# Kernel tuning notes

Hardware: AMD Instinct MI355X
Metric: run time of the kernel (lower is better)

## Reference

```python
import jax, jax.numpy as jnp
import numpy as np

B, M = 4, 32768            # scenes, candidate slots
A = B * (M // 2)           # static number of active points per group
CINS = (64, 128)           # per-group input channels
HID, COUT = 128, 256       # cfg.mlps = [128, 256]
EPS = 1e-5                 # BatchNorm eps


def setup_inputs() -> dict:
    key = jax.random.key(0)
    ks = jax.random.split(key, 12)
    # hard mask: first M//2 columns of every row active -> exactly A True entries
    mask = jnp.tile(jnp.arange(M) < (M // 2), (B, 1))
    inp = {
        "feats0": jax.random.normal(ks[0], (CINS[0], A), jnp.float32),
        "feats1": jax.random.normal(ks[1], (CINS[1], A), jnp.float32),
        "prob0": jax.random.uniform(ks[2], (B, M), jnp.float32),
        "prob1": jax.random.uniform(ks[3], (B, M), jnp.float32),
        "mask0": mask,
        "mask1": mask,
    }
    for g, cin in enumerate(CINS):
        inp[f"Wa{g}"] = jax.random.normal(ks[4 + 2 * g], (HID, cin), jnp.float32) * 0.05
        inp[f"ga{g}"] = jnp.ones((HID,), jnp.float32)
        inp[f"ba{g}"] = jnp.zeros((HID,), jnp.float32)
        inp[f"Wb{g}"] = jax.random.normal(ks[5 + 2 * g], (COUT, HID), jnp.float32) * 0.05
        inp[f"gb{g}"] = jnp.ones((COUT,), jnp.float32)
        inp[f"bb{g}"] = jnp.zeros((COUT,), jnp.float32)
    return inp


def _bn_relu(x, gamma, beta):
    # training-mode BatchNorm1d over the length axis (N=1), biased variance like torch
    mu = x.mean(axis=1, keepdims=True)
    var = x.var(axis=1, keepdims=True)
    y = (x - mu) * jax.lax.rsqrt(var + EPS) * gamma[:, None] + beta[:, None]
    return jax.nn.relu(y)


def _group(feats, prob, mask, Wa, ga, ba, Wb, gb, bb):
    # 1x1 Conv1d == matmul over channels
    h = _bn_relu(Wa @ feats, ga, ba)          # (HID, A)
    y = _bn_relu(Wb @ h, gb, bb)              # (COUT, A)
    # masked scatter into dense (COUT, B*M) zero tensor, row-major like torch bool indexing
    idx = jnp.nonzero(mask.reshape(-1), size=A)[0]
    full = jnp.zeros((COUT, B * M), y.dtype).at[:, idx].set(y)
    # training-time soft-mask weighting by prob, broadcast over channels
    return full.reshape(COUT, B, M) * prob[None]


def reference(feats0, feats1, prob0, prob1, mask0, mask1,
              Wa0, ga0, ba0, Wb0, gb0, bb0,
              Wa1, ga1, ba1, Wb1, gb1, bb1):
    f0 = _group(feats0, prob0, mask0, Wa0, ga0, ba0, Wb0, gb0, bb0)
    f1 = _group(feats1, prob1, mask1, Wa1, ga1, ba1, Wb1, gb1, bb1)
    # sum over groups, then (C,B,M) -> (B,C,M)
    return (f0 + f1).transpose(1, 0, 2)
```

## Files before the change

kernel.cpp:

```cpp
#include <hip/hip_runtime.h>


#define AT 65536

typedef __bf16 bf16_t;
typedef bf16_t bf16x8 __attribute__((ext_vector_type(8)));
typedef bf16_t bf16x4 __attribute__((ext_vector_type(4)));
typedef float  f32x4  __attribute__((ext_vector_type(4)));

__device__ __forceinline__ f32x4 mfma16(bf16x8 a, bf16x8 b, f32x4 c) {
  return __builtin_amdgcn_mfma_f32_16x16x32_bf16(a, b, c, 0, 0, 0);
}

__device__ __forceinline__ float redcol16(float v) {
  v += __shfl_xor(v, 1, 64);
  v += __shfl_xor(v, 2, 64);
  v += __shfl_xor(v, 4, 64);
  v += __shfl_xor(v, 8, 64);
  return v;
}

__device__ __forceinline__ float mux4(const float* v, int sel) {
  float r = v[0];
  r = (sel == 1) ? v[1] : r;
  r = (sel == 2) ? v[2] : r;
  r = (sel == 3) ? v[3] : r;
  return r;
}

__global__ __launch_bounds__(256) void prep_weights(
    const float* __restrict__ Wa0, const float* __restrict__ Wa1,
    const float* __restrict__ Wb0, const float* __restrict__ Wb1,
    bf16_t* __restrict__ Wab0, bf16_t* __restrict__ Wab1,
    bf16_t* __restrict__ Wbb0, bf16_t* __restrict__ Wbb1,
    float* __restrict__ stats)
{
  const int i = threadIdx.x + blockIdx.x * 256;
  if (i < 8192)        Wab0[i]         = (bf16_t)Wa0[i];
  else if (i < 24576)  Wab1[i - 8192]  = (bf16_t)Wa1[i - 8192];
  else if (i < 57344)  Wbb0[i - 24576] = (bf16_t)Wb0[i - 24576];
  else if (i < 90112)  Wbb1[i - 57344] = (bf16_t)Wb1[i - 57344];
  else if (i < 91648)  stats[i - 90112] = 0.f;
}

template <int CIN>
__device__ __forceinline__ void trans_one(
    const float* __restrict__ feats, const bf16_t* __restrict__ Wab,
    float* __restrict__ zsum, float* __restrict__ zssq,
    bf16_t* __restrict__ fT, int blk, char* __restrict__ tile)
{
  constexpr int KS1  = CIN / 32;
  constexpr int GR   = CIN / 8;
  constexpr int ROWB = CIN * 2;
  const int tid = threadIdx.x, lane = tid & 63;
  const int lr = lane & 15, lk = lane >> 4, wid = tid >> 6;
  const int a0 = blk * 64;

  f32x4 v[CIN / 16];
  const int cb = tid >> 4, aq = (tid & 15) * 4;
#pragma unroll
  for (int cc = 0; cc < CIN / 16; ++cc)
    v[cc] = *reinterpret_cast<const f32x4*>(
        feats + (size_t)(cc * 16 + cb) * AT + a0 + aq);

#pragma unroll
  for (int cc = 0; cc < CIN / 16; ++cc) {
    const int c = cc * 16 + cb;
    const int gsw = c >> 3, cbyte = (c & 7) * 2;
#pragma unroll
    for (int i = 0; i < 4; ++i) {
      const int a = aq + i;
      *reinterpret_cast<bf16_t*>(
          tile + a * ROWB + ((gsw ^ (a & 7)) << 4) + cbyte) = (bf16_t)v[cc][i];
    }
  }
  __syncthreads();

  {
    const int g = tid % GR, ar = tid / GR;
#pragma unroll
    for (int i = 0; i < (GR * 64) / 256; ++i) {
      const int a = ar + (256 / GR) * i;
      const bf16x8 w = *reinterpret_cast<const bf16x8*>(
          tile + a * ROWB + ((g ^ (a & 7)) << 4));
      *reinterpret_cast<bf16x8*>(fT + (size_t)(a0 + a) * CIN + g * 8) = w;
    }
  }

  bf16x8 WaF[2][KS1];
#pragma unroll
  for (int mi = 0; mi < 2; ++mi) {
    const bf16_t* base = Wab + (size_t)((2 * wid + mi) * 16 + lr) * CIN + lk * 8;
#pragma unroll
    for (int ks = 0; ks < KS1; ++ks)
      WaF[mi][ks] = *reinterpret_cast<const bf16x8*>(base + ks * 32);
  }

  float zs[2][4] = {}, zq[2][4] = {};
#pragma unroll
  for (int nt = 0; nt < 4; ++nt) {
    const int col = lr + 16 * nt;
    f32x4 z0 = {0.f, 0.f, 0.f, 0.f}, z1 = {0.f, 0.f, 0.f, 0.f};
#pragma unroll
    for (int ks = 0; ks < KS1; ++ks) {
      const int g2 = ks * 4 + lk;
      const bf16x8 bfr = *reinterpret_cast<const bf16x8*>(
          tile + col * ROWB + ((g2 ^ (col & 7)) << 4));
      z0 = mfma16(WaF[0][ks], bfr, z0);
      z1 = mfma16(WaF[1][ks], bfr, z1);
    }
#pragma unroll
    for (int i = 0; i < 4; ++i) {
      zs[0][i] += z0[i]; zq[0][i] += z0[i] * z0[i];
      zs[1][i] += z1[i]; zq[1][i] += z1[i] * z1[i];
    }
  }
#pragma unroll
  for (int mi = 0; mi < 2; ++mi) {
#pragma unroll
    for (int i = 0; i < 4; ++i) {
      zs[mi][i] = redcol16(zs[mi][i]);
      zq[mi][i] = redcol16(zq[mi][i]);
    }
    const float vs = mux4(zs[mi], lr & 3);
    const float vq = mux4(zq[mi], lr & 3);
    const float vv = (lr & 4) ? vq : vs;
    if (lr < 8) {
      const int ch = (2 * wid + mi) * 16 + lk * 4 + (lr & 3);
      atomicAdd(((lr & 4) ? zssq : zsum) + ch, vv);
    }
  }
}

__global__ __launch_bounds__(256) void trans_stats_all(
    const float* __restrict__ feats0, const float* __restrict__ feats1,
    const bf16_t* __restrict__ Wab0, const bf16_t* __restrict__ Wab1,
    float* __restrict__ zsum, float* __restrict__ zssq,
    bf16_t* __restrict__ fT0, bf16_t* __restrict__ fT1)
{
  __shared__ __align__(16) char tile[64 * 256];
  if (blockIdx.x < 1024)
    trans_one<64>(feats0, Wab0, zsum, zssq, fT0, blockIdx.x, tile);
  else
    trans_one<128>(feats1, Wab1, zsum + 128, zssq + 128, fT1,
                   blockIdx.x - 1024, tile);
}

__global__ void finalize_stats(const float* __restrict__ sum,
                               const float* __restrict__ ssq,
                               const float* __restrict__ gamma0,
                               const float* __restrict__ beta0,
                               const float* __restrict__ gamma1,
                               const float* __restrict__ beta1,
                               float* __restrict__ scale,
                               float* __restrict__ shift, int nch)
{
  const int t = threadIdx.x;
  const int g = t / nch;
  const int c = t - g * nch;
  const float inv = 1.f / 65536.f;
  const float mu  = sum[t] * inv;
  const float var = ssq[t] * inv - mu * mu;
  const float ga  = (g ? gamma1 : gamma0)[c];
  const float be  = (g ? beta1 : beta0)[c];
  const float sc  = ga * rsqrtf(var + 1e-5f);
  scale[t] = sc;
  shift[t] = be - mu * sc;
}

template <int CIN>
__device__ __forceinline__ void gemm1_dev(
    const bf16_t* __restrict__ fT, const bf16_t* __restrict__ Wab,
    const float* __restrict__ scZ, const float* __restrict__ shZ,
    char* __restrict__ hw, int colbase, int lr, int lk)
{
  constexpr int KS = CIN / 32;

  bf16x8 bf[2][KS];
#pragma unroll
  for (int sub = 0; sub < 2; ++sub)
#pragma unroll
    for (int ks = 0; ks < KS; ++ks)
      bf[sub][ks] = *reinterpret_cast<const bf16x8*>(
          fT + (size_t)(colbase + sub * 16 + lr) * CIN + lk * 8 + ks * 32);

#pragma unroll 2
  for (int rb = 0; rb < 8; ++rb) {
    bf16x8 af[KS];
    const bf16_t* wa = Wab + (size_t)(rb * 16 + lr) * CIN + lk * 8;
#pragma unroll
    for (int ks = 0; ks < KS; ++ks)
      af[ks] = *reinterpret_cast<const bf16x8*>(wa + ks * 32);

    f32x4 acc[2];
    acc[0] = f32x4{0.f, 0.f, 0.f, 0.f};
    acc[1] = f32x4{0.f, 0.f, 0.f, 0.f};
#pragma unroll
    for (int ks = 0; ks < KS; ++ks) {
      acc[0] = mfma16(af[ks], bf[0][ks], acc[0]);
      acc[1] = mfma16(af[ks], bf[1][ks], acc[1]);
    }

    const f32x4 sv = *reinterpret_cast<const f32x4*>(scZ + rb * 16 + lk * 4);
    const f32x4 bv = *reinterpret_cast<const f32x4*>(shZ + rb * 16 + lk * 4);
#pragma unroll
    for (int sub = 0; sub < 2; ++sub) {
      bf16x4 hv;
#pragma unroll
      for (int i = 0; i < 4; ++i)
        hv[i] = (bf16_t)fmaxf(acc[sub][i] * sv[i] + bv[i], 0.f);
      const int col = sub * 16 + lr;
      const int g8  = rb * 2 + (lk >> 1);
      *reinterpret_cast<bf16x4*>(
          hw + col * 256 + ((g8 ^ (col & 7)) << 4) + ((lk & 1) << 3)) = hv;
    }
  }
}

template <int PHASE>
__global__ __launch_bounds__(256) void fused_pass(
    const bf16_t* __restrict__ fT0, const bf16_t* __restrict__ fT1,
    const bf16_t* __restrict__ Wab0, const bf16_t* __restrict__ Wab1,
    const bf16_t* __restrict__ Wbb0, const bf16_t* __restrict__ Wbb1,
    const float* __restrict__ prob0, const float* __restrict__ prob1,
    const float* __restrict__ scaleZ, const float* __restrict__ shiftZ,
    const float* __restrict__ scaleY, const float* __restrict__ shiftY,
    float* __restrict__ ysum, float* __restrict__ yssq,
    float* __restrict__ out)
{
  __shared__ __align__(16) char hbuf[4][2][8192];
  __shared__ float sstat[(PHASE == 2) ? 1024 : 4];

  const int tid = threadIdx.x, wid = tid >> 6, lane = tid & 63;
  const int lr = lane & 15, lk = lane >> 4;
  const int colbase = (int)blockIdx.x * 128 + wid * 32;

  if constexpr (PHASE == 2) {
    sstat[tid] = 0.f; sstat[tid + 256] = 0.f;
    sstat[tid + 512] = 0.f; sstat[tid + 768] = 0.f;
  }

  gemm1_dev<64>(fT0, Wab0, scaleZ, shiftZ, &hbuf[wid][0][0], colbase, lr, lk);
  gemm1_dev<128>(fT1, Wab1, scaleZ + 128, shiftZ + 128, &hbuf[wid][1][0],
                 colbase, lr, lk);

  if constexpr (PHASE == 2) __syncthreads();

  float p0v[2] = {0.f, 0.f}, p1v[2] = {0.f, 0.f};
  const int bC = (colbase >> 14) * 256;
  const int m0 = colbase & 16383;
  if constexpr (PHASE == 3) {
    const int b = colbase >> 14;
#pragma unroll
    for (int sub = 0; sub < 2; ++sub) {
      const int mm = m0 + sub * 16 + lr;
      p0v[sub] = prob0[((size_t)b << 15) + mm];
      p1v[sub] = prob1[((size_t)b << 15) + mm];
    }
  }

#pragma unroll 2
  for (int rb2 = 0; rb2 < 16; ++rb2) {
    bf16x8 a0f[4], a1f[4];
    const bf16_t* w0 = Wbb0 + (size_t)(rb2 * 16 + lr) * 128 + lk * 8;
    const bf16_t* w1 = Wbb1 + (size_t)(rb2 * 16 + lr) * 128 + lk * 8;
#pragma unroll
    for (int ks = 0; ks < 4; ++ks) {
      a0f[ks] = *reinterpret_cast<const bf16x8*>(w0 + ks * 32);
      a1f[ks] = *reinterpret_cast<const bf16x8*>(w1 + ks * 32);
    }

    f32x4 acc0[2], acc1[2];
    acc0[0] = f32x4{0.f, 0.f, 0.f, 0.f}; acc0[1] = f32x4{0.f, 0.f, 0.f, 0.f};
    acc1[0] = f32x4{0.f, 0.f, 0.f, 0.f}; acc1[1] = f32x4{0.f, 0.f, 0.f, 0.f};
#pragma unroll
    for (int ks2 = 0; ks2 < 4; ++ks2) {
#pragma unroll
      for (int sub = 0; sub < 2; ++sub) {
        const int col = sub * 16 + lr;
        const int off = col * 256 + (((ks2 * 4 + lk) ^ (col & 7)) << 4);
        const bf16x8 h0 = *reinterpret_cast<const bf16x8*>(&hbuf[wid][0][0] + off);
        acc0[sub] = mfma16(a0f[ks2], h0, acc0[sub]);
        const bf16x8 h1 = *reinterpret_cast<const bf16x8*>(&hbuf[wid][1][0] + off);
        acc1[sub] = mfma16(a1f[ks2], h1, acc1[sub]);
      }
    }

    if constexpr (PHASE == 2) {
#pragma unroll
      for (int g = 0; g < 2; ++g) {
        const f32x4* ac = g ? acc1 : acc0;
        float s[4], q[4];
#pragma unroll
        for (int i = 0; i < 4; ++i) {
          s[i] = redcol16(ac[0][i] + ac[1][i]);
          q[i] = redcol16(ac[0][i] * ac[0][i] + ac[1][i] * ac[1][i]);
        }
        const float vs = mux4(s, lr & 3);
        const float vq = mux4(q, lr & 3);
        const float vv = (lr & 4) ? vq : vs;
        if (lr < 8)
          atomicAdd(&sstat[g * 512 + ((lr >> 2) << 8) +
                           rb2 * 16 + lk * 4 + (lr & 3)], vv);
      }
    } else {
      const f32x4 sv0 = *reinterpret_cast<const f32x4*>(scaleY + rb2 * 16 + lk * 4);
      const f32x4 bv0 = *reinterpret_cast<const f32x4*>(shiftY + rb2 * 16 + lk * 4);
      const f32x4 sv1 = *reinterpret_cast<const f32x4*>(scaleY + 256 + rb2 * 16 + lk * 4);
      const f32x4 bv1 = *reinterpret_cast<const f32x4*>(shiftY + 256 + rb2 * 16 + lk * 4);
#pragma unroll
      for (int sub = 0; sub < 2; ++sub) {
        const int mm = m0 + sub * 16 + lr;
#pragma unroll
        for (int i = 0; i < 4; ++i) {
          const int ch = rb2 * 16 + lk * 4 + i;
          const float v =
              fmaxf(acc0[sub][i] * sv0[i] + bv0[i], 0.f) * p0v[sub] +
              fmaxf(acc1[sub][i] * sv1[i] + bv1[i], 0.f) * p1v[sub];
          float* op = out + (((size_t)(bC + ch)) << 15) + mm;
          op[0] = v;
          op[16384] = 0.f;
        }
      }
    }
  }

  if constexpr (PHASE == 2) {
    __syncthreads();
#pragma unroll
    for (int j = 0; j < 4; ++j) {
      const int g = j >> 1, sq = j & 1;
      atomicAdd((sq ? yssq : ysum) + g * 256 + tid,
                sstat[g * 512 + sq * 256 + tid]);
    }
  }
}

extern "C" void kernel_launch(void* const* d_in, const int* in_sizes, int n_in,
                              void* d_out, int out_size, void* d_ws, size_t ws_size,
                              hipStream_t stream)
{
  (void)in_sizes; (void)n_in; (void)out_size; (void)ws_size;
  const float* feats0 = (const float*)d_in[0];
  const float* feats1 = (const float*)d_in[1];
  const float* prob0  = (const float*)d_in[2];
  const float* prob1  = (const float*)d_in[3];
  const float* Wa0 = (const float*)d_in[6];
  const float* ga0 = (const float*)d_in[7];
  const float* ba0 = (const float*)d_in[8];
  const float* Wb0 = (const float*)d_in[9];
  const float* gb0 = (const float*)d_in[10];
  const float* bb0 = (const float*)d_in[11];
  const float* Wa1 = (const float*)d_in[12];
  const float* ga1 = (const float*)d_in[13];
  const float* ba1 = (const float*)d_in[14];
  const float* Wb1 = (const float*)d_in[15];
  const float* gb1 = (const float*)d_in[16];
  const float* bb1 = (const float*)d_in[17];

  float* out = (float*)d_out;
  char*  wsb = (char*)d_ws;
  float* ws  = (float*)d_ws;

  float* zsum = ws;
  float* zssq = ws + 256;
  float* ysum = ws + 512;
  float* yssq = ws + 1024;
  float* scaleZ = ws + 1536;
  float* shiftZ = ws + 1792;
  float* scaleY = ws + 2048;
  float* shiftY = ws + 2560;
  bf16_t* Wab0 = (bf16_t*)(wsb + (16  << 10));
  bf16_t* Wab1 = (bf16_t*)(wsb + (32  << 10));
  bf16_t* Wbb0 = (bf16_t*)(wsb + (64  << 10));
  bf16_t* Wbb1 = (bf16_t*)(wsb + (128 << 10));
  bf16_t* fT0 = (bf16_t*)(wsb + (256 << 10));
  bf16_t* fT1 = (bf16_t*)(wsb + (256 << 10) + (8 << 20));

  prep_weights<<<358, 256, 0, stream>>>(Wa0, Wa1, Wb0, Wb1,
                                        Wab0, Wab1, Wbb0, Wbb1, zsum);

  trans_stats_all<<<2048, 256, 0, stream>>>(feats0, feats1, Wab0, Wab1,
                                            zsum, zssq, fT0, fT1);

  finalize_stats<<<1, 256, 0, stream>>>(zsum, zssq, ga0, ba0, ga1, ba1,
                                        scaleZ, shiftZ, 128);

  fused_pass<2><<<512, 256, 0, stream>>>(fT0, fT1, Wab0, Wab1, Wbb0, Wbb1,
      prob0, prob1, scaleZ, shiftZ, scaleY, shiftY, ysum, yssq, out);

  finalize_stats<<<1, 512, 0, stream>>>(ysum, yssq, gb0, bb0, gb1, bb1,
                                        scaleY, shiftY, 256);

  fused_pass<3><<<512, 256, 0, stream>>>(fT0, fT1, Wab0, Wab1, Wbb0, Wbb1,
      prob0, prob1, scaleZ, shiftZ, scaleY, shiftY, ysum, yssq, out);
}
```

Measured before the change: 204.8 us.

## Replace atomic BN stat accumulation with per-block partials and vectorize output stores

Per-block batch-norm sums and squared sums are now written to workspace partial buffers instead of atomically added to global accumulators. New parallel reduce_fin kernels (one wave per channel) reduce those partials and compute scale and shift. This removes global atomic contention and the zero-init of the stats. Separately, columns are remapped so each lane owns two adjacent positions. That allows float2 loads of prob and float2 stores of the output and its zero half. The cost is extra workspace traffic for the partials and more reduction blocks.

Result: faster. 170.9 us (-16.5%).

```diff
diff --git a/kernel.cpp b/kernel.cpp
--- a/kernel.cpp
+++ b/kernel.cpp
@@ -7,6 +7,7 @@
 typedef bf16_t bf16x8 __attribute__((ext_vector_type(8)));
 typedef bf16_t bf16x4 __attribute__((ext_vector_type(4)));
 typedef float  f32x4  __attribute__((ext_vector_type(4)));
+typedef float  f32x2  __attribute__((ext_vector_type(2)));
 
 __device__ __forceinline__ f32x4 mfma16(bf16x8 a, bf16x8 b, f32x4 c) {
   return __builtin_amdgcn_mfma_f32_16x16x32_bf16(a, b, c, 0, 0, 0);
@@ -32,22 +33,20 @@
     const float* __restrict__ Wa0, const float* __restrict__ Wa1,
     const float* __restrict__ Wb0, const float* __restrict__ Wb1,
     bf16_t* __restrict__ Wab0, bf16_t* __restrict__ Wab1,
-    bf16_t* __restrict__ Wbb0, bf16_t* __restrict__ Wbb1,
-    float* __restrict__ stats)
+    bf16_t* __restrict__ Wbb0, bf16_t* __restrict__ Wbb1)
 {
   const int i = threadIdx.x + blockIdx.x * 256;
   if (i < 8192)        Wab0[i]         = (bf16_t)Wa0[i];
   else if (i < 24576)  Wab1[i - 8192]  = (bf16_t)Wa1[i - 8192];
   else if (i < 57344)  Wbb0[i - 24576] = (bf16_t)Wb0[i - 24576];
   else if (i < 90112)  Wbb1[i - 57344] = (bf16_t)Wb1[i - 57344];
-  else if (i < 91648)  stats[i - 90112] = 0.f;
 }
 
 template <int CIN>
 __device__ __forceinline__ void trans_one(
     const float* __restrict__ feats, const bf16_t* __restrict__ Wab,
-    float* __restrict__ zsum, float* __restrict__ zssq,
-    bf16_t* __restrict__ fT, int blk, char* __restrict__ tile)
+    float* __restrict__ Zpart_blk, bf16_t* __restrict__ fT,
+    int blk, char* __restrict__ tile)
 {
   constexpr int KS1  = CIN / 32;
   constexpr int GR   = CIN / 8;
@@ -127,7 +126,7 @@
     const float vv = (lr & 4) ? vq : vs;
     if (lr < 8) {
       const int ch = (2 * wid + mi) * 16 + lk * 4 + (lr & 3);
-      atomicAdd(((lr & 4) ? zssq : zsum) + ch, vv);
+      Zpart_blk[((lr & 4) ? 128 : 0) + ch] = vv;
     }
   }
 }
@@ -135,37 +134,51 @@
 __global__ __launch_bounds__(256) void trans_stats_all(
     const float* __restrict__ feats0, const float* __restrict__ feats1,
     const bf16_t* __restrict__ Wab0, const bf16_t* __restrict__ Wab1,
-    float* __restrict__ zsum, float* __restrict__ zssq,
+    float* __restrict__ Zpart,
     bf16_t* __restrict__ fT0, bf16_t* __restrict__ fT1)
 {
   __shared__ __align__(16) char tile[64 * 256];
+  float* zp = Zpart + (size_t)blockIdx.x * 256;
   if (blockIdx.x < 1024)
-    trans_one<64>(feats0, Wab0, zsum, zssq, fT0, blockIdx.x, tile);
+    trans_one<64>(feats0, Wab0, zp, fT0, blockIdx.x, tile);
   else
-    trans_one<128>(feats1, Wab1, zsum + 128, zssq + 128, fT1,
-                   blockIdx.x - 1024, tile);
-}
-
-__global__ void finalize_stats(const float* __restrict__ sum,
-                               const float* __restrict__ ssq,
-                               const float* __restrict__ gamma0,
-                               const float* __restrict__ beta0,
-                               const float* __restrict__ gamma1,
-                               const float* __restrict__ beta1,
-                               float* __restrict__ scale,
-                               float* __restrict__ shift, int nch)
-{
+    trans_one<128>(feats1, Wab1, zp, fT1, blockIdx.x - 1024, tile);
+}
+
+__global__ void reduce_fin(const float* __restrict__ part,
+                           long grp_stride, int blk_stride, int nblk, int nch,
+                           const float* __restrict__ gamma0,
+                           const float* __restrict__ beta0,
+                           const float* __restrict__ gamma1,
+                           const float* __restrict__ beta1,
+                           float* __restrict__ scale,
+                           float* __restrict__ shift)
+{
+  const int bid = blockIdx.x;
+  const int g = bid >= nch ? 1 : 0;
+  const int c = bid - g * nch;
   const int t = threadIdx.x;
-  const int g = t / nch;
-  const int c = t - g * nch;
-  const float inv = 1.f / 65536.f;
-  const float mu  = sum[t] * inv;
-  const float var = ssq[t] * inv - mu * mu;
-  const float ga  = (g ? gamma1 : gamma0)[c];
-  const float be  = (g ? beta1 : beta0)[c];
-  const float sc  = ga * rsqrtf(var + 1e-5f);
-  scale[t] = sc;
-  shift[t] = be - mu * sc;
+  const float* p = part + (size_t)g * grp_stride;
+  float s = 0.f, q = 0.f;
+  for (int b = t; b < nblk; b += 64) {
+    s += p[(size_t)b * blk_stride + c];
+    q += p[(size_t)b * blk_stride + nch + c];
+  }
+#pragma unroll
+  for (int o = 1; o < 64; o <<= 1) {
+    s += __shfl_xor(s, o, 64);
+    q += __shfl_xor(q, o, 64);
+  }
+  if (t == 0) {
+    const float inv = 1.f / 65536.f;
+    const float mu  = s * inv;
+    const float var = q * inv - mu * mu;
+    const float ga  = (g ? gamma1 : gamma0)[c];
+    const float be  = (g ? beta1 : beta0)[c];
+    const float sc  = ga * rsqrtf(var + 1e-5f);
+    scale[g * nch + c] = sc;
+    shift[g * nch + c] = be - mu * sc;
+  }
 }
 
 template <int CIN>
@@ -178,11 +191,11 @@
 
   bf16x8 bf[2][KS];
 #pragma unroll
-  for (int sub = 0; sub < 2; ++sub)
+  for (int nt = 0; nt < 2; ++nt)
 #pragma unroll
     for (int ks = 0; ks < KS; ++ks)
-      bf[sub][ks] = *reinterpret_cast<const bf16x8*>(
-          fT + (size_t)(colbase + sub * 16 + lr) * CIN + lk * 8 + ks * 32);
+      bf[nt][ks] = *reinterpret_cast<const bf16x8*>(
+          fT + (size_t)(colbase + lr * 2 + nt) * CIN + lk * 8 + ks * 32);
 
 #pragma unroll 2
   for (int rb = 0; rb < 8; ++rb) {
@@ -204,15 +217,15 @@
     const f32x4 sv = *reinterpret_cast<const f32x4*>(scZ + rb * 16 + lk * 4);
     const f32x4 bv = *reinterpret_cast<const f32x4*>(shZ + rb * 16 + lk * 4);
 #pragma unroll
-    for (int sub = 0; sub < 2; ++sub) {
+    for (int nt = 0; nt < 2; ++nt) {
       bf16x4 hv;
 #pragma unroll
       for (int i = 0; i < 4; ++i)
-        hv[i] = (bf16_t)fmaxf(acc[sub][i] * sv[i] + bv[i], 0.f);
-      const int col = sub * 16 + lr;
-      const int g8  = rb * 2 + (lk >> 1);
+        hv[i] = (bf16_t)fmaxf(acc[nt][i] * sv[i] + bv[i], 0.f);
+      const int s = nt * 16 + lr;
+      const int g8 = rb * 2 + (lk >> 1);
       *reinterpret_cast<bf16x4*>(
-          hw + col * 256 + ((g8 ^ (col & 7)) << 4) + ((lk & 1) << 3)) = hv;
+          hw + s * 256 + ((g8 ^ (s & 7)) << 4) + ((lk & 1) << 3)) = hv;
     }
   }
 }
@@ -225,8 +238,7 @@
     const float* __restrict__ prob0, const float* __restrict__ prob1,
     const float* __restrict__ scaleZ, const float* __restrict__ shiftZ,
     const float* __restrict__ scaleY, const float* __restrict__ shiftY,
-    float* __restrict__ ysum, float* __restrict__ yssq,
-    float* __restrict__ out)
+    float* __restrict__ Ypart, float* __restrict__ out)
 {
   __shared__ __align__(16) char hbuf[4][2][8192];
   __shared__ float sstat[(PHASE == 2) ? 1024 : 4];
@@ -246,17 +258,13 @@
 
   if constexpr (PHASE == 2) __syncthreads();
 
-  float p0v[2] = {0.f, 0.f}, p1v[2] = {0.f, 0.f};
+  f32x2 p0v = {0.f, 0.f}, p1v = {0.f, 0.f};
   const int bC = (colbase >> 14) * 256;
   const int m0 = colbase & 16383;
   if constexpr (PHASE == 3) {
     const int b = colbase >> 14;
-#pragma unroll
-    for (int sub = 0; sub < 2; ++sub) {
-      const int mm = m0 + sub * 16 + lr;
-      p0v[sub] = prob0[((size_t)b << 15) + mm];
-      p1v[sub] = prob1[((size_t)b << 15) + mm];
-    }
+    p0v = *reinterpret_cast<const f32x2*>(prob0 + ((size_t)b << 15) + m0 + lr * 2);
+    p1v = *reinterpret_cast<const f32x2*>(prob1 + ((size_t)b << 15) + m0 + lr * 2);
   }
 
 #pragma unroll 2
@@ -276,13 +284,13 @@
 #pragma unroll
     for (int ks2 = 0; ks2 < 4; ++ks2) {
 #pragma unroll
-      for (int sub = 0; sub < 2; ++sub) {
-        const int col = sub * 16 + lr;
-        const int off = col * 256 + (((ks2 * 4 + lk) ^ (col & 7)) << 4);
+      for (int nt = 0; nt < 2; ++nt) {
+        const int s = nt * 16 + lr;
+        const int off = s * 256 + (((ks2 * 4 + lk) ^ (s & 7)) << 4);
         const bf16x8 h0 = *reinterpret_cast<const bf16x8*>(&hbuf[wid][0][0] + off);
-        acc0[sub] = mfma16(a0f[ks2], h0, acc0[sub]);
+        acc0[nt] = mfma16(a0f[ks2], h0, acc0[nt]);
         const bf16x8 h1 = *reinterpret_cast<const bf16x8*>(&hbuf[wid][1][0] + off);
-        acc1[sub] = mfma16(a1f[ks2], h1, acc1[sub]);
+        acc1[nt] = mfma16(a1f[ks2], h1, acc1[nt]);
       }
     }
 
@@ -308,19 +316,18 @@
       const f32x4 bv0 = *reinterpret_cast<const f32x4*>(shiftY + rb2 * 16 + lk * 4);
       const f32x4 sv1 = *reinterpret_cast<const f32x4*>(scaleY + 256 + rb2 * 16 + lk * 4);
       const f32x4 bv1 = *reinterpret_cast<const f32x4*>(shiftY + 256 + rb2 * 16 + lk * 4);
-#pragma unroll
-      for (int sub = 0; sub < 2; ++sub) {
-        const int mm = m0 + sub * 16 + lr;
-#pragma unroll
-        for (int i = 0; i < 4; ++i) {
-          const int ch = rb2 * 16 + lk * 4 + i;
-          const float v =
-              fmaxf(acc0[sub][i] * sv0[i] + bv0[i], 0.f) * p0v[sub] +
-              fmaxf(acc1[sub][i] * sv1[i] + bv1[i], 0.f) * p1v[sub];
-          float* op = out + (((size_t)(bC + ch)) << 15) + mm;
-          op[0] = v;
-          op[16384] = 0.f;
-        }
+      const f32x2 zz = {0.f, 0.f};
+#pragma unroll
+      for (int i = 0; i < 4; ++i) {
+        const int ch = rb2 * 16 + lk * 4 + i;
+        f32x2 w;
+#pragma unroll
+        for (int nt = 0; nt < 2; ++nt)
+          w[nt] = fmaxf(acc0[nt][i] * sv0[i] + bv0[i], 0.f) * p0v[nt] +
+                  fmaxf(acc1[nt][i] * sv1[i] + bv1[i], 0.f) * p1v[nt];
+        float* op = out + (((size_t)(bC + ch)) << 15) + m0 + lr * 2;
+        *reinterpret_cast<f32x2*>(op) = w;
+        *reinterpret_cast<f32x2*>(op + 16384) = zz;
       }
     }
   }
@@ -328,11 +335,8 @@
   if constexpr (PHASE == 2) {
     __syncthreads();
 #pragma unroll
-    for (int j = 0; j < 4; ++j) {
-      const int g = j >> 1, sq = j & 1;
-      atomicAdd((sq ? yssq : ysum) + g * 256 + tid,
-                sstat[g * 512 + sq * 256 + tid]);
-    }
+    for (int j = 0; j < 4; ++j)
+      Ypart[(size_t)blockIdx.x * 1024 + j * 256 + tid] = sstat[j * 256 + tid];
   }
 }
 
@@ -362,36 +366,34 @@
   char*  wsb = (char*)d_ws;
   float* ws  = (float*)d_ws;
 
-  float* zsum = ws;
-  float* zssq = ws + 256;
-  float* ysum = ws + 512;
-  float* yssq = ws + 1024;
-  float* scaleZ = ws + 1536;
-  float* shiftZ = ws + 1792;
-  float* scaleY = ws + 2048;
-  float* shiftY = ws + 2560;
+  float* scaleZ = ws;
+  float* shiftZ = ws + 256;
+  float* scaleY = ws + 512;
+  float* shiftY = ws + 1024;
   bf16_t* Wab0 = (bf16_t*)(wsb + (16  << 10));
   bf16_t* Wab1 = (bf16_t*)(wsb + (32  << 10));
   bf16_t* Wbb0 = (bf16_t*)(wsb + (64  << 10));
   bf16_t* Wbb1 = (bf16_t*)(wsb + (128 << 10));
-  bf16_t* fT0 = (bf16_t*)(wsb + (256 << 10));
-  bf16_t* fT1 = (bf16_t*)(wsb + (256 << 10) + (8 << 20));
-
-  prep_weights<<<358, 256, 0, stream>>>(Wa0, Wa1, Wb0, Wb1,
-                                        Wab0, Wab1, Wbb0, Wbb1, zsum);
+  float* Zpart = (float*)(wsb + (256 << 10));
+  float* Ypart = (float*)(wsb + (2560 << 10));
+  bf16_t* fT0 = (bf16_t*)(wsb + (8ull  << 20));
+  bf16_t* fT1 = (bf16_t*)(wsb + (16ull << 20));
+
+  prep_weights<<<352, 256, 0, stream>>>(Wa0, Wa1, Wb0, Wb1,
+                                        Wab0, Wab1, Wbb0, Wbb1);
 
   trans_stats_all<<<2048, 256, 0, stream>>>(feats0, feats1, Wab0, Wab1,
-                                            zsum, zssq, fT0, fT1);
-
-  finalize_stats<<<1, 256, 0, stream>>>(zsum, zssq, ga0, ba0, ga1, ba1,
-                                        scaleZ, shiftZ, 128);
+                                            Zpart, fT0, fT1);
+
+  reduce_fin<<<256, 64, 0, stream>>>(Zpart, 1024L * 256, 256, 1024, 128,
+                                     ga0, ba0, ga1, ba1, scaleZ, shiftZ);
 
   fused_pass<2><<<512, 256, 0, stream>>>(fT0, fT1, Wab0, Wab1, Wbb0, Wbb1,
-      prob0, prob1, scaleZ, shiftZ, scaleY, shiftY, ysum, yssq, out);
-
-  finalize_stats<<<1, 512, 0, stream>>>(ysum, yssq, gb0, bb0, gb1, bb1,
-                                        scaleY, shiftY, 256);
+      prob0, prob1, scaleZ, shiftZ, scaleY, shiftY, Ypart, out);
+
+  reduce_fin<<<512, 64, 0, stream>>>(Ypart, 512L, 1024, 512, 256,
+                                     gb0, bb0, gb1, bb1, scaleY, shiftY);
 
   fused_pass<3><<<512, 256, 0, stream>>>(fT0, fT1, Wab0, Wab1, Wbb0, Wbb1,
-      prob0, prob1, scaleZ, shiftZ, scaleY, shiftY, ysum, yssq, out);
-}
+      prob0, prob1, scaleZ, shiftZ, scaleY, shiftY, Ypart, out);
+}
```
